# Performance work log

Hardware: AMD Instinct MI355X
Metric: run time of the kernel (lower is better)

The kernel has to match this reference:

```python
import jax, jax.numpy as jnp
import numpy as np

N_ENT = 100000
N_REL = 200          # -> 2*N_REL = 400 edge types
D = 128
NB = 4               # num_bases (hard-coded in MGCN)
E = 800000


def _rgcn_conv(x, src, dst, edge_type, edge_norm, basis, att, root, bias):
    # x: [N, D]; basis: [NB, D, D]; att: [2R, NB]; root: [D, D]; bias: [D]
    n = x.shape[0]
    x_j = x[src]                      # [E, D] gather source node feats
    att_e = att[edge_type]            # [E, NB] per-edge basis coefficients
    # message: x_j @ (sum_b att_e[b] * basis_b), computed basis-wise to avoid
    # materializing [E, D, D] per-edge weights (same math as gather+bmm)
    msg = att_e[:, 0:1] * (x_j @ basis[0])
    for b in range(1, NB):
        msg = msg + att_e[:, b:b+1] * (x_j @ basis[b])
    msg = msg * edge_norm[:, None]
    # mean aggregation into target nodes (zeros for isolated nodes)
    agg = jax.ops.segment_sum(msg, dst, num_segments=n)
    cnt = jax.ops.segment_sum(jnp.ones_like(edge_norm), dst, num_segments=n)
    agg = agg / jnp.maximum(cnt, 1.0)[:, None]
    return agg + x @ root + bias


def setup_inputs() -> dict:
    key = jax.random.key(0)
    ks = jax.random.split(key, 16)
    s = 1.0 / np.sqrt(NB * D)  # uniform init scale as in reset_parameters
    inp = {
        "entity": jnp.arange(N_ENT, dtype=jnp.int32),
        "edge_index": jax.random.randint(ks[0], (2, E), 0, N_ENT, dtype=jnp.int32),
        "edge_type": jax.random.randint(ks[1], (E,), 0, 2 * N_REL, dtype=jnp.int32),
        "edge_norm": jax.random.uniform(ks[2], (E,), dtype=jnp.float32),
        "emb": jax.random.normal(ks[3], (N_ENT, D), dtype=jnp.float32),
        "basis1": jax.random.uniform(ks[4], (NB, D, D), dtype=jnp.float32, minval=-s, maxval=s),
        "att1": jax.random.uniform(ks[5], (2 * N_REL, NB), dtype=jnp.float32, minval=-s, maxval=s),
        "root1": jax.random.uniform(ks[6], (D, D), dtype=jnp.float32, minval=-s, maxval=s),
        "bias1": jax.random.uniform(ks[7], (D,), dtype=jnp.float32, minval=-s, maxval=s),
        "basis2": jax.random.uniform(ks[8], (NB, D, D), dtype=jnp.float32, minval=-s, maxval=s),
        "att2": jax.random.uniform(ks[9], (2 * N_REL, NB), dtype=jnp.float32, minval=-s, maxval=s),
        "root2": jax.random.uniform(ks[10], (D, D), dtype=jnp.float32, minval=-s, maxval=s),
        "bias2": jax.random.uniform(ks[11], (D,), dtype=jnp.float32, minval=-s, maxval=s),
    }
    return inp


def reference(entity, edge_index, edge_type, edge_norm, emb,
              basis1, att1, root1, bias1, basis2, att2, root2, bias2):
    src, dst = edge_index[0], edge_index[1]
    x = emb[entity]  # [N, D]
    # forward applies conv1 TWICE (as in the original code), then conv2;
    # dropout is identity in eval mode
    x = _rgcn_conv(x, src, dst, edge_type, edge_norm, basis1, att1, root1, bias1)
    x = jax.nn.relu(_rgcn_conv(x, src, dst, edge_type, edge_norm, basis1, att1, root1, bias1))
    x = _rgcn_conv(x, src, dst, edge_type, edge_norm, basis2, att2, root2, bias2)
    return x
```

## Files before the change

kernel.cpp:

```cpp
#include <hip/hip_runtime.h>

#define D 128
#define NB 4
#define BM2 256
#define SCAN_B 1024

typedef unsigned short u16;
typedef unsigned int u32;
using bf16x8 = __attribute__((ext_vector_type(8))) short;
using f32x4  = __attribute__((ext_vector_type(4))) float;

__device__ __forceinline__ float bf2f(u16 u) {
    union { u32 i; float f; } v; v.i = ((u32)u) << 16; return v.f;
}
__device__ __forceinline__ u16 f2bf(float f) {
    union { float ff; u32 i; } v; v.ff = f;
    u32 r = v.i + 0x7fffu + ((v.i >> 16) & 1u);
    return (u16)(r >> 16);
}

__device__ __forceinline__ void async16(void* lds, const void* g) {
    __builtin_amdgcn_global_load_lds(
        (const __attribute__((address_space(1))) unsigned int*)g,
        (__attribute__((address_space(3))) unsigned int*)lds,
        16, 0, 0);
}


__global__ __launch_bounds__(256) void degree_int_kernel(const int* __restrict__ dst,
                                                         int* __restrict__ deg, int E) {
    int e = blockIdx.x * 256 + threadIdx.x;
    if (e < E) atomicAdd(&deg[dst[e]], 1);
}

__global__ __launch_bounds__(256) void scan1_kernel(const int* __restrict__ deg,
                                                    int* __restrict__ row_start,
                                                    int* __restrict__ bsum, int n) {
    __shared__ int tsum[256];
    int base = blockIdx.x * SCAN_B;
    int t = threadIdx.x;
    int v[4];
    int s = 0;
#pragma unroll
    for (int i = 0; i < 4; ++i) {
        int idx = base + t * 4 + i;
        v[i] = (idx < n) ? deg[idx] : 0;
        s += v[i];
    }
    tsum[t] = s;
    __syncthreads();
    for (int off = 1; off < 256; off <<= 1) {
        int x = (t >= off) ? tsum[t - off] : 0;
        __syncthreads();
        tsum[t] += x;
        __syncthreads();
    }
    int run = tsum[t] - s;
#pragma unroll
    for (int i = 0; i < 4; ++i) {
        int idx = base + t * 4 + i;
        if (idx < n) row_start[idx] = run;
        run += v[i];
    }
    if (t == 255) bsum[blockIdx.x] = tsum[255];
}

__global__ __launch_bounds__(256) void scan2_kernel(int* __restrict__ bsum, int nb) {
    __shared__ int buf[256];
    __shared__ int carry_s;
    if (threadIdx.x == 0) carry_s = 0;
    __syncthreads();
    for (int base = 0; base < nb; base += 256) {
        int i = base + threadIdx.x;
        int v = (i < nb) ? bsum[i] : 0;
        buf[threadIdx.x] = v;
        __syncthreads();
        for (int off = 1; off < 256; off <<= 1) {
            int x = (threadIdx.x >= (unsigned)off) ? buf[threadIdx.x - off] : 0;
            __syncthreads();
            buf[threadIdx.x] += x;
            __syncthreads();
        }
        if (i < nb) bsum[i] = carry_s + buf[threadIdx.x] - v;
        __syncthreads();
        if (threadIdx.x == 0) carry_s += buf[255];
        __syncthreads();
    }
}

__global__ __launch_bounds__(256) void scan3_kernel(const int* __restrict__ deg,
                                                    const int* __restrict__ bsum,
                                                    int* __restrict__ row_start,
                                                    float* __restrict__ inv, int n, int E) {
    int i = blockIdx.x * 256 + threadIdx.x;
    if (i < n) {
        row_start[i] += bsum[i >> 10];
        inv[i] = 1.0f / fmaxf((float)deg[i], 1.0f);
    }
    if (i == 0) row_start[n] = E;
}

__global__ __launch_bounds__(256) void fill_kernel(
    const int* __restrict__ src, const int* __restrict__ dst,
    const int* __restrict__ row_start, int* __restrict__ fill,
    int2* __restrict__ csr_se, int E)
{
    int e = blockIdx.x * 256 + threadIdx.x;
    if (e >= E) return;
    int d0 = dst[e];
    int pos = row_start[d0] + atomicAdd(&fill[d0], 1);
    csr_se[pos] = make_int2(src[e], e);
}

__global__ __launch_bounds__(256) void coef_kernel(
    const int2* __restrict__ csr_se, const int* __restrict__ etype,
    const float* __restrict__ norm, const float* __restrict__ att,
    float4* __restrict__ csr_coef, int E)
{
    int p = blockIdx.x * 256 + threadIdx.x;
    if (p >= E) return;
    int e = csr_se[p].y;
    float nm = norm[e];
    float4 a = ((const float4*)att)[etype[e]];
    csr_coef[p] = make_float4(a.x * nm, a.y * nm, a.z * nm, a.w * nm);
}


__global__ __launch_bounds__(256) void tobf_gather_kernel(const int* __restrict__ entity,
                                                          const float* __restrict__ emb,
                                                          u16* __restrict__ xbf, int n) {
    int idx = blockIdx.x * 256 + threadIdx.x;
    if (idx >= n * 32) return;
    int row = idx >> 5, c = idx & 31;
    float4 v = ((const float4*)emb)[(size_t)entity[row] * 32 + c];
    ushort4 o;
    o.x = f2bf(v.x); o.y = f2bf(v.y); o.z = f2bf(v.z); o.w = f2bf(v.w);
    ((ushort4*)xbf)[idx] = o;
}

#define AGG_BODY(UJ)                                                            \
    {                                                                           \
        float4 c = c_[UJ];                                                      \
        float4 xv;                                                              \
        xv.x = bf2f(u_[UJ].x); xv.y = bf2f(u_[UJ].y);                           \
        xv.z = bf2f(u_[UJ].z); xv.w = bf2f(u_[UJ].w);                           \
        z0.x += c.x * xv.x; z0.y += c.x * xv.y; z0.z += c.x * xv.z; z0.w += c.x * xv.w; \
        z1.x += c.y * xv.x; z1.y += c.y * xv.y; z1.z += c.y * xv.z; z1.w += c.y * xv.w; \
        z2.x += c.z * xv.x; z2.y += c.z * xv.y; z2.z += c.z * xv.z; z2.w += c.z * xv.w; \
        z3.x += c.w * xv.x; z3.y += c.w * xv.y; z3.z += c.w * xv.z; z3.w += c.w * xv.w; \
    }

__global__ __launch_bounds__(256) void agg_kernel(
    const int* __restrict__ row_start, const int* __restrict__ deg,
    const float* __restrict__ inv, const int2* __restrict__ csr_se,
    const float4* __restrict__ csr_coef, const u16* __restrict__ xbf,
    u16* __restrict__ Zbf, int n)
{
    int nd = blockIdx.x * 8 + (threadIdx.x >> 5);
    if (nd >= n) return;
    int q = threadIdx.x & 31;
    int s0 = row_start[nd];
    int dg = deg[nd];
    float4 z0 = make_float4(0.f,0.f,0.f,0.f), z1 = z0, z2 = z0, z3 = z0;

    int i = 0;
    for (; i + 8 <= dg; i += 8) {
        int s_[8]; float4 c_[8]; ushort4 u_[8];
#pragma unroll
        for (int j = 0; j < 8; ++j) s_[j] = csr_se[s0 + i + j].x;
#pragma unroll
        for (int j = 0; j < 8; ++j) c_[j] = csr_coef[s0 + i + j];
#pragma unroll
        for (int j = 0; j < 8; ++j) u_[j] = ((const ushort4*)xbf)[(size_t)s_[j] * 32 + q];
#pragma unroll
        for (int j = 0; j < 8; ++j) AGG_BODY(j)
    }
    for (; i + 4 <= dg; i += 4) {
        int s_[4]; float4 c_[4]; ushort4 u_[4];
#pragma unroll
        for (int j = 0; j < 4; ++j) s_[j] = csr_se[s0 + i + j].x;
#pragma unroll
        for (int j = 0; j < 4; ++j) c_[j] = csr_coef[s0 + i + j];
#pragma unroll
        for (int j = 0; j < 4; ++j) u_[j] = ((const ushort4*)xbf)[(size_t)s_[j] * 32 + q];
#pragma unroll
        for (int j = 0; j < 4; ++j) AGG_BODY(j)
    }
    for (; i < dg; ++i) {
        int s_[1]; float4 c_[1]; ushort4 u_[1];
        s_[0] = csr_se[s0 + i].x;
        c_[0] = csr_coef[s0 + i];
        u_[0] = ((const ushort4*)xbf)[(size_t)s_[0] * 32 + q];
        AGG_BODY(0)
    }

    float iv = inv[nd];
    ushort4* zp = ((ushort4*)Zbf) + (size_t)nd * 128;
    ushort4 o;
    o.x = f2bf(z0.x * iv); o.y = f2bf(z0.y * iv); o.z = f2bf(z0.z * iv); o.w = f2bf(z0.w * iv);
    zp[q] = o;
    o.x = f2bf(z1.x * iv); o.y = f2bf(z1.y * iv); o.z = f2bf(z1.z * iv); o.w = f2bf(z1.w * iv);
    zp[32 + q] = o;
    o.x = f2bf(z2.x * iv); o.y = f2bf(z2.y * iv); o.z = f2bf(z2.z * iv); o.w = f2bf(z2.w * iv);
    zp[64 + q] = o;
    o.x = f2bf(z3.x * iv); o.y = f2bf(z3.y * iv); o.z = f2bf(z3.z * iv); o.w = f2bf(z3.w * iv);
    zp[96 + q] = o;
}

__global__ __launch_bounds__(256) void wprep_kernel(
    const float* __restrict__ basis, const float* __restrict__ root,
    u16* __restrict__ Wt)
{
    int idx = blockIdx.x * 256 + threadIdx.x;
    if (idx >= 640 * 128) return;
    int k = idx >> 7, nn = idx & 127;
    float w = (k < 512) ? basis[(size_t)k * 128 + nn] : root[(size_t)(k - 512) * 128 + nn];
    u16 hi = f2bf(w);
    float lo = w - bf2f(hi);
    Wt[(size_t)nn * 1280 + k] = hi;
    Wt[(size_t)nn * 1280 + 640 + k] = f2bf(lo);
}

__global__ __launch_bounds__(512) void mfma_gemm_kernel(
    const u16* __restrict__ Zbf, const u16* __restrict__ xbf,
    const u16* __restrict__ Wt, const float* __restrict__ bias,
    int relu, int write_bf, u16* __restrict__ obf, float* __restrict__ of32, int n)
{
    __shared__ u16 As[BM2 * 64];
    __shared__ u16 Bh[128 * 64];
    __shared__ u16 Bl[128 * 64];

    const int tid  = threadIdx.x;
    const int row0 = blockIdx.x * BM2;
    const int lane = tid & 63;
    const int w    = tid >> 6;
    const int wr   = (w >> 1) * 64;
    const int wc   = (w & 1) * 64;
    const int lr   = lane & 15;
    const int lk   = lane >> 4;

    const int srow = lane >> 3;
    const int sswz = ((lane & 7) * 16) ^ (srow << 4);

    f32x4 zero = {0.f, 0.f, 0.f, 0.f};
    f32x4 acc[4][4];
#pragma unroll
    for (int mi = 0; mi < 4; ++mi)
#pragma unroll
        for (int ni = 0; ni < 4; ++ni) acc[mi][ni] = zero;

    for (int c = 0; c < 10; ++c) {
        const int wk = c * 64;
        __syncthreads();
#pragma unroll
        for (int j = 0; j < 4; ++j) {
            int r    = (w << 5) + (j << 3) + srow;
            int grow = row0 + r;
            const u16* gp = (c < 8)
                ? (Zbf + (size_t)grow * 512 + wk)
                : (xbf + (size_t)grow * 128 + (c - 8) * 64);
            async16((char*)As + (((w << 5) + (j << 3)) << 7),
                    (const char*)gp + sswz);
        }
#pragma unroll
        for (int j = 0; j < 2; ++j) {
            int rr = (w << 4) + (j << 3) + srow;
            const u16* gp = Wt + (size_t)rr * 1280 + wk;
            async16((char*)Bh + (((w << 4) + (j << 3)) << 7),
                    (const char*)gp + sswz);
            async16((char*)Bl + (((w << 4) + (j << 3)) << 7),
                    (const char*)(gp + 640) + sswz);
        }
        __syncthreads();

#pragma unroll
        for (int kh = 0; kh < 2; ++kh) {
            const int kb = (kh * 64 + lk * 16) ^ ((lr & 7) << 4);
            bf16x8 af[4], bh[4], bl[4];
#pragma unroll
            for (int mi = 0; mi < 4; ++mi)
                af[mi] = *(const bf16x8*)((const char*)As + ((wr + mi * 16 + lr) << 7) + kb);
#pragma unroll
            for (int ni = 0; ni < 4; ++ni)
                bh[ni] = *(const bf16x8*)((const char*)Bh + ((wc + ni * 16 + lr) << 7) + kb);
#pragma unroll
            for (int mi = 0; mi < 4; ++mi)
#pragma unroll
                for (int ni = 0; ni < 4; ++ni)
                    acc[mi][ni] = __builtin_amdgcn_mfma_f32_16x16x32_bf16(
                        af[mi], bh[ni], acc[mi][ni], 0, 0, 0);
#pragma unroll
            for (int ni = 0; ni < 4; ++ni)
                bl[ni] = *(const bf16x8*)((const char*)Bl + ((wc + ni * 16 + lr) << 7) + kb);
#pragma unroll
            for (int mi = 0; mi < 4; ++mi)
#pragma unroll
                for (int ni = 0; ni < 4; ++ni)
                    acc[mi][ni] = __builtin_amdgcn_mfma_f32_16x16x32_bf16(
                        af[mi], bl[ni], acc[mi][ni], 0, 0, 0);
        }
    }

#pragma unroll
    for (int ni = 0; ni < 4; ++ni) {
        int col = wc + ni * 16 + lr;
        float bv = bias[col];
#pragma unroll
        for (int mi = 0; mi < 4; ++mi) {
#pragma unroll
            for (int r = 0; r < 4; ++r) {
                int row = row0 + wr + mi * 16 + lk * 4 + r;
                if (row < n) {
                    float v = acc[mi][ni][r] + bv;
                    if (relu) v = fmaxf(v, 0.f);
                    if (write_bf) obf[(size_t)row * 128 + col] = f2bf(v);
                    else          of32[(size_t)row * 128 + col] = v;
                }
            }
        }
    }
}


extern "C" void kernel_launch(void* const* d_in, const int* in_sizes, int n_in,
                              void* d_out, int out_size, void* d_ws, size_t ws_size,
                              hipStream_t stream) {
    const int*   entity     = (const int*)d_in[0];
    const int*   edge_index = (const int*)d_in[1];
    const int*   edge_type  = (const int*)d_in[2];
    const float* edge_norm  = (const float*)d_in[3];
    const float* emb        = (const float*)d_in[4];
    const float* basis1     = (const float*)d_in[5];
    const float* att1       = (const float*)d_in[6];
    const float* root1      = (const float*)d_in[7];
    const float* bias1      = (const float*)d_in[8];
    const float* basis2     = (const float*)d_in[9];
    const float* att2       = (const float*)d_in[10];
    const float* root2      = (const float*)d_in[11];
    const float* bias2      = (const float*)d_in[12];
    float* out = (float*)d_out;

    const int N = in_sizes[0];
    const int E = in_sizes[2];
    const int* src = edge_index;
    const int* dst = edge_index + E;

    size_t ND = (size_t)N * D;
    char* wp = (char*)d_ws;
    int nb = (N + SCAN_B - 1) / SCAN_B;

    size_t off = 0;
    u16*    Zbf      = (u16*)(wp + off);   off += ND * 8;
    u16*    xbf0     = (u16*)(wp + off);   off += ND * 2;
    u16*    Wt       = (u16*)(wp + off);   off += (size_t)128 * 1280 * 2;
    float4* csr_coef = (float4*)(wp + off); off += (size_t)E * 16;
    int2*   csr_se   = (int2*)(wp + off);  off += (size_t)E * 8;
    int*    deg      = (int*)(wp + off);   off += (size_t)N * 4;
    int*    fill     = (int*)(wp + off);   off += (size_t)N * 4;
    float*  inv      = (float*)(wp + off); off += (size_t)N * 4;
    int*    row_start= (int*)(wp + off);   off += (size_t)(N + 1) * 4;
    int*    bsum     = (int*)(wp + off);   off += (size_t)(nb + 1) * 4;
    size_t need = off;

    if (ws_size < need) {
        hipMemsetAsync(d_out, 0, (size_t)out_size * sizeof(float), stream);
        return;
    }

    u16* xbf1 = (u16*)d_out;

    int eblk = (E + 255) / 256;
    int ablk = (N + 7) / 8;
    int gblk = (N * 32 + 255) / 256;
    int mblk = (N + BM2 - 1) / BM2;
    int wblk = (640 * 128 + 255) / 256;
    int nblk256 = (N + 255) / 256;

    hipMemsetAsync(deg, 0, (size_t)N * 4, stream);
    degree_int_kernel<<<eblk, 256, 0, stream>>>(dst, deg, E);
    scan1_kernel<<<nb, 256, 0, stream>>>(deg, row_start, bsum, N);
    scan2_kernel<<<1, 256, 0, stream>>>(bsum, nb);
    scan3_kernel<<<nblk256, 256, 0, stream>>>(deg, bsum, row_start, inv, N, E);
    hipMemsetAsync(fill, 0, (size_t)N * 4, stream);
    fill_kernel<<<eblk, 256, 0, stream>>>(src, dst, row_start, fill, csr_se, E);
    coef_kernel<<<eblk, 256, 0, stream>>>(csr_se, edge_type, edge_norm, att1, csr_coef, E);
    tobf_gather_kernel<<<gblk, 256, 0, stream>>>(entity, emb, xbf0, N);
    wprep_kernel<<<wblk, 256, 0, stream>>>(basis1, root1, Wt);

    agg_kernel<<<ablk, 256, 0, stream>>>(row_start, deg, inv, csr_se, csr_coef, xbf0, Zbf, N);
    mfma_gemm_kernel<<<mblk, 512, 0, stream>>>(Zbf, xbf0, Wt, bias1, 0, 1, xbf1, nullptr, N);

    agg_kernel<<<ablk, 256, 0, stream>>>(row_start, deg, inv, csr_se, csr_coef, xbf1, Zbf, N);
    mfma_gemm_kernel<<<mblk, 512, 0, stream>>>(Zbf, xbf1, Wt, bias1, 1, 1, xbf0, nullptr, N);

    coef_kernel<<<eblk, 256, 0, stream>>>(csr_se, edge_type, edge_norm, att2, csr_coef, E);
    wprep_kernel<<<wblk, 256, 0, stream>>>(basis2, root2, Wt);
    agg_kernel<<<ablk, 256, 0, stream>>>(row_start, deg, inv, csr_se, csr_coef, xbf0, Zbf, N);
    mfma_gemm_kernel<<<mblk, 512, 0, stream>>>(Zbf, xbf0, Wt, bias2, 0, 0, nullptr, out, N);
}
```

Before: 518.0 us.

## Double-buffer LDS tiles in MFMA GEMM with async prefetch of next K-chunk

The GEMM kernel now keeps two LDS buffers for the A and B tiles. It issues async global-to-LDS loads for chunk c+1 before computing chunk c, and waits on vmcnt so only the current chunk's loads must be done. The hi and lo weight halves are merged into one swizzled 128-wide B tile per stage. The aim is to hide global load latency behind the MFMA work. The cost is doubled LDS use (about 128KB per block), which likely cuts occupancy to one block per CU.

```diff
diff --git a/kernel.cpp b/kernel.cpp
--- a/kernel.cpp
+++ b/kernel.cpp
@@ -2,7 +2,7 @@
 
 #define D 128
 #define NB 4
-#define BM2 256
+#define BMP 256
 #define SCAN_B 1024
 
 typedef unsigned short u16;
@@ -226,12 +226,11 @@
     const u16* __restrict__ Wt, const float* __restrict__ bias,
     int relu, int write_bf, u16* __restrict__ obf, float* __restrict__ of32, int n)
 {
-    __shared__ u16 As[BM2 * 64];
-    __shared__ u16 Bh[128 * 64];
-    __shared__ u16 Bl[128 * 64];
+    __shared__ u16 As[2][BMP * 64];
+    __shared__ u16 Bs[2][128 * 128];
 
     const int tid  = threadIdx.x;
-    const int row0 = blockIdx.x * BM2;
+    const int row0 = blockIdx.x * BMP;
     const int lane = tid & 63;
     const int w    = tid >> 6;
     const int wr   = (w >> 1) * 64;
@@ -239,8 +238,11 @@
     const int lr   = lane & 15;
     const int lk   = lane >> 4;
 
-    const int srow = lane >> 3;
-    const int sswz = ((lane & 7) * 16) ^ (srow << 4);
+    const int srowA = lane >> 3;
+    const int sswzA = ((lane & 7) << 4) ^ (srowA << 4);
+    const int srowB = lane >> 4;
+    const int halfB = (lane >> 3) & 1;
+    const int slotB = (lane & 7) << 4;
 
     f32x4 zero = {0.f, 0.f, 0.f, 0.f};
     f32x4 acc[4][4];
@@ -249,40 +251,48 @@
 #pragma unroll
         for (int ni = 0; ni < 4; ++ni) acc[mi][ni] = zero;
 
+    auto STAGE = [&](int c, int p) {
+#pragma unroll
+        for (int j = 0; j < 4; ++j) {
+            int r    = (w << 5) + (j << 3) + srowA;
+            int grow = row0 + r;
+            const char* gp = (c < 8)
+                ? (const char*)(Zbf + (size_t)grow * 512 + c * 64)
+                : (const char*)(xbf + (size_t)grow * 128 + (c - 8) * 64);
+            async16((char*)&As[p][((w << 5) + (j << 3)) * 64], gp + sswzA);
+        }
+#pragma unroll
+        for (int j = 0; j < 4; ++j) {
+            int rr = (w << 4) + (j << 2) + srowB;
+            const char* gp = (const char*)Wt + (size_t)rr * 2560
+                           + (halfB ? 1280 : 0) + c * 128
+                           + (slotB ^ ((rr & 7) << 4));
+            async16((char*)&Bs[p][((w << 4) + (j << 2)) * 128], gp);
+        }
+    };
+
+    STAGE(0, 0);
+
     for (int c = 0; c < 10; ++c) {
-        const int wk = c * 64;
-        __syncthreads();
-#pragma unroll
-        for (int j = 0; j < 4; ++j) {
-            int r    = (w << 5) + (j << 3) + srow;
-            int grow = row0 + r;
-            const u16* gp = (c < 8)
-                ? (Zbf + (size_t)grow * 512 + wk)
-                : (xbf + (size_t)grow * 128 + (c - 8) * 64);
-            async16((char*)As + (((w << 5) + (j << 3)) << 7),
-                    (const char*)gp + sswz);
-        }
-#pragma unroll
-        for (int j = 0; j < 2; ++j) {
-            int rr = (w << 4) + (j << 3) + srow;
-            const u16* gp = Wt + (size_t)rr * 1280 + wk;
-            async16((char*)Bh + (((w << 4) + (j << 3)) << 7),
-                    (const char*)gp + sswz);
-            async16((char*)Bl + (((w << 4) + (j << 3)) << 7),
-                    (const char*)(gp + 640) + sswz);
-        }
-        __syncthreads();
+        const int p = c & 1;
+        if (c < 9) STAGE(c + 1, p ^ 1);
+        __builtin_amdgcn_sched_barrier(0);
+        if (c < 9) asm volatile("s_waitcnt vmcnt(8)" ::: "memory");
+        else       asm volatile("s_waitcnt vmcnt(0)" ::: "memory");
+        __builtin_amdgcn_sched_barrier(0);
+        __builtin_amdgcn_s_barrier();
+        __builtin_amdgcn_sched_barrier(0);
 
 #pragma unroll
         for (int kh = 0; kh < 2; ++kh) {
-            const int kb = (kh * 64 + lk * 16) ^ ((lr & 7) << 4);
+            const int kb = ((kh * 4 + lk) << 4) ^ ((lr & 7) << 4);
             bf16x8 af[4], bh[4], bl[4];
 #pragma unroll
             for (int mi = 0; mi < 4; ++mi)
-                af[mi] = *(const bf16x8*)((const char*)As + ((wr + mi * 16 + lr) << 7) + kb);
+                af[mi] = *(const bf16x8*)((const char*)&As[p][0] + (wr + mi * 16 + lr) * 128 + kb);
 #pragma unroll
             for (int ni = 0; ni < 4; ++ni)
-                bh[ni] = *(const bf16x8*)((const char*)Bh + ((wc + ni * 16 + lr) << 7) + kb);
+                bh[ni] = *(const bf16x8*)((const char*)&Bs[p][0] + (wc + ni * 16 + lr) * 256 + kb);
 #pragma unroll
             for (int mi = 0; mi < 4; ++mi)
 #pragma unroll
@@ -291,7 +301,7 @@
                         af[mi], bh[ni], acc[mi][ni], 0, 0, 0);
 #pragma unroll
             for (int ni = 0; ni < 4; ++ni)
-                bl[ni] = *(const bf16x8*)((const char*)Bl + ((wc + ni * 16 + lr) << 7) + kb);
+                bl[ni] = *(const bf16x8*)((const char*)&Bs[p][0] + (wc + ni * 16 + lr) * 256 + 128 + kb);
 #pragma unroll
             for (int mi = 0; mi < 4; ++mi)
 #pragma unroll
@@ -299,6 +309,9 @@
                     acc[mi][ni] = __builtin_amdgcn_mfma_f32_16x16x32_bf16(
                         af[mi], bl[ni], acc[mi][ni], 0, 0, 0);
         }
+        __builtin_amdgcn_sched_barrier(0);
+        __builtin_amdgcn_s_barrier();
+        __builtin_amdgcn_sched_barrier(0);
     }
 
 #pragma unroll
@@ -372,7 +385,7 @@
     int eblk = (E + 255) / 256;
     int ablk = (N + 7) / 8;
     int gblk = (N * 32 + 255) / 256;
-    int mblk = (N + BM2 - 1) / BM2;
+    int mblk = (N + BMP - 1) / BMP;
     int wblk = (640 * 128 + 255) / 256;
     int nblk256 = (N + 255) / 256;
 
```

New measurement: 506.1 us. -2.3%, faster.
